# Optimization experiments

Hardware: AMD Instinct MI355X
Metric: run time of the kernel (lower is better)

The kernel has to match this reference:

```python
import jax, jax.numpy as jnp
import numpy as np

V, E, H, L = 10000, 300, 256, 9   # vocab, embed_dim, hidden_dim, num_labels
B, T = 128, 512                   # batch, seq_len


def setup_inputs() -> dict:
    key = jax.random.key(0)
    ks = jax.random.split(key, 14)
    s = 0.05
    emb = jax.random.normal(ks[2], (V, E), jnp.float32) * s
    emb = emb.at[0].set(0.0)  # padding_idx=0
    return {
        "input_ids": jax.random.randint(ks[0], (B, T), 0, V),
        "attention_mask": jnp.ones((B, T), jnp.int32),
        "labels": jax.random.randint(ks[1], (B, T), 0, L),
        "emb": emb,
        "Wih_f": jax.random.normal(ks[3], (4 * H, E), jnp.float32) * s,
        "Whh_f": jax.random.normal(ks[4], (4 * H, H), jnp.float32) * s,
        "b_f": jnp.zeros((4 * H,), jnp.float32),
        "Wih_b": jax.random.normal(ks[5], (4 * H, E), jnp.float32) * s,
        "Whh_b": jax.random.normal(ks[6], (4 * H, H), jnp.float32) * s,
        "b_b": jnp.zeros((4 * H,), jnp.float32),
        "Wc": jax.random.normal(ks[7], (L, 2 * H), jnp.float32) * s,
        "bc": jnp.zeros((L,), jnp.float32),
        "transitions": jax.random.normal(ks[8], (L, L), jnp.float32) * 0.1,
        "start_trans": jax.random.normal(ks[9], (L,), jnp.float32) * 0.1,
        "end_trans": jax.random.normal(ks[10], (L,), jnp.float32) * 0.1,
    }


def _lstm_dir(x, Wih, Whh, b):
    # x: (T, B, E) -> hidden states (T, B, H); PyTorch gate order i,f,g,o
    Bn = x.shape[1]
    h0 = jnp.zeros((Bn, Whh.shape[1]), x.dtype)
    c0 = jnp.zeros((Bn, Whh.shape[1]), x.dtype)
    # precompute input projections once (big GEMM), scan only does small HxH GEMM
    xp = jnp.einsum('tbe,ge->tbg', x, Wih) + b
    def step(carry, xg):
        h, c = carry
        g = xg + h @ Whh.T
        i, f, gg, o = jnp.split(g, 4, axis=-1)
        c = jax.nn.sigmoid(f) * c + jax.nn.sigmoid(i) * jnp.tanh(gg)
        h = jax.nn.sigmoid(o) * jnp.tanh(c)
        return (h, c), h
    _, hs = jax.lax.scan(step, (h0, c0), xp)
    return hs


def reference(input_ids, attention_mask, labels, emb, Wih_f, Whh_f, b_f,
              Wih_b, Whh_b, b_b, Wc, bc, transitions, start_trans, end_trans):
    x = emb[input_ids]                       # (B, T, E)
    xt = jnp.transpose(x, (1, 0, 2))         # (T, B, E)
    hf = _lstm_dir(xt, Wih_f, Whh_f, b_f)
    hb = _lstm_dir(xt[::-1], Wih_b, Whh_b, b_b)[::-1]
    h = jnp.concatenate([hf, hb], axis=-1)   # (T, B, 2H); dropout is identity in eval
    em = h @ Wc.T + bc                       # (T, B, L) emissions

    mask = jnp.transpose(attention_mask, (1, 0)).astype(bool)  # (T, B)
    tags = jnp.transpose(labels, (1, 0))                        # (T, B)
    Bn = em.shape[1]
    bidx = jnp.arange(Bn)

    # --- numerator: score of gold path (torchcrf._compute_score) ---
    score0 = start_trans[tags[0]] + em[0, bidx, tags[0]]
    def num_step(carry, inp):
        score, prev = carry
        e_t, t_t, m_t = inp
        score = score + (transitions[prev, t_t] + e_t[bidx, t_t]) * m_t
        return (score, t_t), None
    (score, _), _ = jax.lax.scan(
        num_step, (score0, tags[0]),
        (em[1:], tags[1:], mask[1:].astype(em.dtype)))
    seq_ends = mask.astype(jnp.int32).sum(0) - 1
    last_tags = tags[seq_ends, bidx]
    score = score + end_trans[last_tags]

    # --- denominator: log partition (torchcrf._compute_normalizer) ---
    alpha0 = start_trans + em[0]             # (B, L)
    def den_step(alpha, inp):
        e_t, m_t = inp
        nxt = jax.nn.logsumexp(alpha[:, :, None] + transitions[None] + e_t[:, None, :], axis=1)
        return jnp.where(m_t[:, None], nxt, alpha), None
    alpha, _ = jax.lax.scan(den_step, alpha0, (em[1:], mask[1:]))
    logZ = jax.nn.logsumexp(alpha + end_trans, axis=-1)

    llh = score - logZ
    return -jnp.mean(llh)  # crf(..., reduction='mean'), negated
```

## Files before the change

kernel.cpp:

```cpp
#include <hip/hip_runtime.h>
#include <hip/hip_bf16.h>
#include <hip/hip_fp16.h>

#define Vn 10000
#define En 300
#define E2n 150
#define Hn 256
#define Gn 1024
#define Ln 9
#define Bn 128
#define Tn 512

#if defined(__has_builtin)
#  if __has_builtin(__builtin_amdgcn_sdot8)
#    define HAS_SDOT8 1
#  endif
#endif
#ifndef HAS_SDOT8
#  define HAS_SDOT8 0
#endif

typedef _Float16 half2_t __attribute__((ext_vector_type(2)));

static __device__ __forceinline__ float bf2f(unsigned short u) {
    return __uint_as_float(((unsigned int)u) << 16);
}
static __device__ __forceinline__ unsigned short f2bf(float f) {
    unsigned int x = __float_as_uint(f);
    return (unsigned short)((x + 0x7FFFu + ((x >> 16) & 1u)) >> 16);
}
static __device__ __forceinline__ float sigm(float x) {
    return 1.f / (1.f + __expf(-x));
}
static __device__ __forceinline__ float tanh_fast(float x) {
    return 2.f / (1.f + __expf(-2.f * x)) - 1.f;
}
static __device__ __forceinline__ int dot8(unsigned int w, int h, int acc) {
#if HAS_SDOT8
    return __builtin_amdgcn_sdot8((int)w, h, acc, false);
#else
    unsigned int wl = ((w & 0x0F0F0F0Fu) ^ 0x08080808u) - 0x08080808u;
    unsigned int wh = (((w >> 4) & 0x0F0F0F0Fu) ^ 0x08080808u) - 0x08080808u;
    unsigned int hl = (((unsigned)h & 0x0F0F0F0Fu) ^ 0x08080808u) - 0x08080808u;
    unsigned int hh = ((((unsigned)h >> 4) & 0x0F0F0F0Fu) ^ 0x08080808u) - 0x08080808u;
    acc = __builtin_amdgcn_sdot4((int)wl, (int)hl, acc, false);
    return __builtin_amdgcn_sdot4((int)wh, (int)hh, acc, false);
#endif
}
static __device__ __forceinline__ unsigned int packf16(float a, float b) {
    half2_t v = {(_Float16)a, (_Float16)b};
    return __builtin_bit_cast(unsigned int, v);
}
static __device__ __forceinline__ half2_t h2(unsigned int u) {
    return __builtin_bit_cast(half2_t, u);
}

#define NPREP_A 5860
#define NPREP_B 1200
#define NPREP_C 512

__global__ __launch_bounds__(256) void k_prep(
    const float* __restrict__ emb, unsigned int* __restrict__ embp,
    const float* __restrict__ Wih_f, const float* __restrict__ Wih_b,
    unsigned int* __restrict__ WT16_f, unsigned int* __restrict__ WT16_b,
    const float* __restrict__ Whh_f, const float* __restrict__ Whh_b,
    unsigned int* __restrict__ qr_f, unsigned int* __restrict__ ql_f,
    unsigned int* __restrict__ qr_b, unsigned int* __restrict__ ql_b,
    float* __restrict__ scl_f, float* __restrict__ scl_b) {
    int bx = blockIdx.x, tid = threadIdx.x;
    if (bx < NPREP_A) {
        int n = bx * 256 + tid;
        if (n < Vn * E2n) {
            int v = n / E2n, e2 = n % E2n;
            embp[n] = packf16(emb[(size_t)v * En + 2 * e2],
                              emb[(size_t)v * En + 2 * e2 + 1]);
        }
        return;
    }
    if (bx < NPREP_A + NPREP_B) {
        int m = (bx - NPREP_A) * 256 + tid;
        int dir = m / 153600;
        int n = m % 153600;
        const float* src = dir ? Wih_b : Wih_f;
        unsigned int* dst = dir ? WT16_b : WT16_f;
        int e2 = n / Gn, j = n % Gn;
        dst[n] = packf16(src[(size_t)j * En + 2 * e2],
                         src[(size_t)j * En + 2 * e2 + 1]);
        return;
    }
    int idx = (bx - NPREP_A - NPREP_B) * 4 + (tid >> 6);
    int dir = idx >> 10;
    int j = idx & 1023;
    int lane = tid & 63;
    const float* W = dir ? Whh_b : Whh_f;
    float w8[8];
    float m = 0.f;
    if (lane < 32) {
        float4 wlo = *(const float4*)&W[(size_t)j * Hn + 8 * lane];
        float4 whi = *(const float4*)&W[(size_t)j * Hn + 8 * lane + 4];
        w8[0] = wlo.x; w8[1] = wlo.y; w8[2] = wlo.z; w8[3] = wlo.w;
        w8[4] = whi.x; w8[5] = whi.y; w8[6] = whi.z; w8[7] = whi.w;
        #pragma unroll
        for (int i = 0; i < 8; ++i) m = fmaxf(m, fabsf(w8[i]));
    }
    #pragma unroll
    for (int sft = 32; sft >= 1; sft >>= 1) m = fmaxf(m, __shfl_xor(m, sft, 64));
    float inv = (m > 0.f) ? (7.f / m) : 0.f;
    if (lane < 32) {
        unsigned int d = 0;
        #pragma unroll
        for (int i = 0; i < 8; ++i) {
            int qi = (int)rintf(w8[i] * inv);
            d |= ((unsigned int)(qi & 0xF)) << (4 * i);
        }
        if (lane < 24)
            (dir ? qr_b : qr_f)[(size_t)((lane >> 2) * 1024 + j) * 4 + (lane & 3)] = d;
        else {
            int e = lane - 24;
            (dir ? ql_b : ql_f)[(size_t)((e >> 2) * 1024 + j) * 4 + (e & 3)] = d;
        }
    }
    if (lane == 0) (dir ? scl_b : scl_f)[j] = m / 49.f;
}

__global__ __launch_bounds__(256) void k_proj(
    const unsigned int* __restrict__ embp,
    const unsigned int* __restrict__ WT16_f, const unsigned int* __restrict__ WT16_b,
    const float* __restrict__ b_f, const float* __restrict__ b_b,
    unsigned short* __restrict__ Pf, unsigned short* __restrict__ Pb) {
    int tid = threadIdx.x;
    int tx = tid & 63, ty = tid >> 6;
    int dir = blockIdx.z;
    const unsigned int* WT = dir ? WT16_b : WT16_f;
    const float* bias = dir ? b_b : b_f;
    unsigned short* P = dir ? Pb : Pf;
    int v0 = blockIdx.x * 32 + ty * 8;
    int j0 = blockIdx.y * 256 + tx * 4;
    int vr[8];
    #pragma unroll
    for (int r = 0; r < 8; ++r) { int v = v0 + r; vr[r] = (v < Vn) ? v : Vn - 1; }
    half2_t ax[8], ay[8], az[8], aw[8];
    #pragma unroll
    for (int r = 0; r < 8; ++r) {
        half2_t z = {(_Float16)0.f, (_Float16)0.f};
        ax[r] = z; ay[r] = z; az[r] = z; aw[r] = z;
    }
    for (int e2 = 0; e2 < E2n; e2 += 2) {
        uint4 w0 = *(const uint4*)&WT[(size_t)(e2 + 0) * Gn + j0];
        uint4 w1 = *(const uint4*)&WT[(size_t)(e2 + 1) * Gn + j0];
        #pragma unroll
        for (int r = 0; r < 8; ++r) {
            uint2 a = *(const uint2*)&embp[(size_t)vr[r] * E2n + e2];
            half2_t a0 = h2(a.x), a1 = h2(a.y);
            ax[r] += a0 * h2(w0.x); ay[r] += a0 * h2(w0.y);
            az[r] += a0 * h2(w0.z); aw[r] += a0 * h2(w0.w);
            ax[r] += a1 * h2(w1.x); ay[r] += a1 * h2(w1.y);
            az[r] += a1 * h2(w1.z); aw[r] += a1 * h2(w1.w);
        }
    }
    float4 bb = *(const float4*)&bias[j0];
    #pragma unroll
    for (int r = 0; r < 8; ++r) {
        if (v0 + r < Vn) {
            ushort4 o;
            o.x = f2bf((float)ax[r].x + (float)ax[r].y + bb.x);
            o.y = f2bf((float)ay[r].x + (float)ay[r].y + bb.y);
            o.z = f2bf((float)az[r].x + (float)az[r].y + bb.z);
            o.w = f2bf((float)aw[r].x + (float)aw[r].y + bb.w);
            *(ushort4*)&P[(size_t)(v0 + r) * Gn + j0] = o;
        }
    }
}

__global__ __launch_bounds__(1024, 4) void k_lstm(
    const int* __restrict__ ids,
    const uint4* __restrict__ qr_f, const uint4* __restrict__ ql_f,
    const uint4* __restrict__ qr_b, const uint4* __restrict__ ql_b,
    const float* __restrict__ scl_f, const float* __restrict__ scl_b,
    const unsigned short* __restrict__ Pf, const unsigned short* __restrict__ Pb,
    unsigned short* __restrict__ hs_f, unsigned short* __restrict__ hs_b) {
    __shared__ uint4 wlds[2 * 1024];
    __shared__ float g_stage[Gn];
    __shared__ uint4 h4v[8];
    __shared__ int ids_lds[Tn];
    int tid = threadIdx.x;
    int dir = blockIdx.x >> 7;
    int batch = blockIdx.x & 127;
    const uint4* qr = dir ? qr_b : qr_f;
    const uint4* ql = dir ? ql_b : ql_f;
    const unsigned short* P = dir ? Pb : Pf;
    unsigned short* hs = dir ? hs_b : hs_f;

    unsigned int wReg[24];
    #pragma unroll
    for (int d4 = 0; d4 < 6; ++d4) {
        uint4 v = qr[(size_t)d4 * 1024 + tid];
        wReg[4*d4+0] = v.x; wReg[4*d4+1] = v.y; wReg[4*d4+2] = v.z; wReg[4*d4+3] = v.w;
    }
    wlds[tid] = ql[tid];
    wlds[1024 + tid] = ql[1024 + tid];
    float sc = (dir ? scl_b : scl_f)[tid];
    if (tid < Tn) ids_lds[tid] = ids[batch * Tn + tid];
    if (tid < 8) { uint4 z = {0u, 0u, 0u, 0u}; h4v[tid] = z; }
    float c = 0.f;
    __syncthreads();

    int t0 = dir ? (Tn - 1) : 0;
    float p = bf2f(P[(size_t)ids_lds[t0] * Gn + tid]);

    for (int s = 0; s < Tn; ++s) {
        asm volatile("" : "+v"(wReg[0]), "+v"(wReg[1]), "+v"(wReg[2]), "+v"(wReg[3]),
                          "+v"(wReg[4]), "+v"(wReg[5]), "+v"(wReg[6]), "+v"(wReg[7]),
                          "+v"(wReg[8]), "+v"(wReg[9]), "+v"(wReg[10]), "+v"(wReg[11]));
        asm volatile("" : "+v"(wReg[12]), "+v"(wReg[13]), "+v"(wReg[14]), "+v"(wReg[15]),
                          "+v"(wReg[16]), "+v"(wReg[17]), "+v"(wReg[18]), "+v"(wReg[19]),
                          "+v"(wReg[20]), "+v"(wReg[21]), "+v"(wReg[22]), "+v"(wReg[23]));

        int t = dir ? (Tn - 1 - s) : s;
        int s2 = (s + 1 < Tn) ? s + 1 : Tn - 1;
        int t2 = dir ? (Tn - 1 - s2) : s2;
        unsigned short nx = P[(size_t)ids_lds[t2] * Gn + tid];

        uint4 hq  = h4v[tid & 7];
        uint4 wv0 = wlds[tid];
        uint4 wv1 = wlds[1024 + tid];

        int a0 = 0, a1 = 0, a2 = 0, a3 = 0;
        #pragma unroll
        for (int g = 0; g < 6; ++g) {
            int h0 = __builtin_amdgcn_readlane((int)hq.x, g);
            int h1 = __builtin_amdgcn_readlane((int)hq.y, g);
            int h2v = __builtin_amdgcn_readlane((int)hq.z, g);
            int h3 = __builtin_amdgcn_readlane((int)hq.w, g);
            a0 = dot8(wReg[4*g+0], h0, a0);
            a1 = dot8(wReg[4*g+1], h1, a1);
            a2 = dot8(wReg[4*g+2], h2v, a2);
            a3 = dot8(wReg[4*g+3], h3, a3);
        }
        {
            int h0 = __builtin_amdgcn_readlane((int)hq.x, 6);
            int h1 = __builtin_amdgcn_readlane((int)hq.y, 6);
            int h2v = __builtin_amdgcn_readlane((int)hq.z, 6);
            int h3 = __builtin_amdgcn_readlane((int)hq.w, 6);
            a0 = dot8(wv0.x, h0, a0);
            a1 = dot8(wv0.y, h1, a1);
            a2 = dot8(wv0.z, h2v, a2);
            a3 = dot8(wv0.w, h3, a3);
            h0 = __builtin_amdgcn_readlane((int)hq.x, 7);
            h1 = __builtin_amdgcn_readlane((int)hq.y, 7);
            h2v = __builtin_amdgcn_readlane((int)hq.z, 7);
            h3 = __builtin_amdgcn_readlane((int)hq.w, 7);
            a0 = dot8(wv1.x, h0, a0);
            a1 = dot8(wv1.y, h1, a1);
            a2 = dot8(wv1.z, h2v, a2);
            a3 = dot8(wv1.w, h3, a3);
        }
        g_stage[tid] = sc * (float)((a0 + a1) + (a2 + a3)) + p;
        __syncthreads();
        if (tid < Hn) {
            float gi = g_stage[tid];
            float gf = g_stage[tid + 256];
            float gg = g_stage[tid + 512];
            float go = g_stage[tid + 768];
            float cn = sigm(gf) * c + sigm(gi) * tanh_fast(gg);
            float hn = sigm(go) * tanh_fast(cn);
            c = cn;
            hs[(size_t)(t * Bn + batch) * Hn + tid] = f2bf(hn);
            int qh = (int)rintf(7.f * hn);
            int qo = __shfl_xor(qh, 1, 64);
            if ((tid & 1) == 0)
                ((char*)h4v)[tid >> 1] = (char)((qh & 0xF) | ((qo & 0xF) << 4));
        }
        __syncthreads();
        p = bf2f(nx);
    }
}

__global__ __launch_bounds__(256) void k_emit(
    const unsigned short* __restrict__ hs_f, const unsigned short* __restrict__ hs_b,
    const float* __restrict__ Wc, const float* __restrict__ bc,
    float* __restrict__ em) {
    __shared__ float wc_s[Ln * 2 * Hn];
    int tid = threadIdx.x;
    for (int i = tid; i < Ln * 2 * Hn; i += 256) wc_s[i] = Wc[i];
    __syncthreads();
    int lane = tid & 63, wid = tid >> 6;
    int tb0 = blockIdx.x * 16 + wid * 4;
    for (int i = 0; i < 4; ++i) {
        int tb = tb0 + i;
        const unsigned short* hf = hs_f + (size_t)tb * Hn;
        const unsigned short* hb = hs_b + (size_t)tb * Hn;
        uint2 uf = *(const uint2*)&hf[lane * 4];
        uint2 ub = *(const uint2*)&hb[lane * 4];
        float f0 = __uint_as_float(uf.x << 16), f1 = __uint_as_float(uf.x & 0xFFFF0000u);
        float f2v = __uint_as_float(uf.y << 16), f3 = __uint_as_float(uf.y & 0xFFFF0000u);
        float b0 = __uint_as_float(ub.x << 16), b1 = __uint_as_float(ub.x & 0xFFFF0000u);
        float b2 = __uint_as_float(ub.y << 16), b3 = __uint_as_float(ub.y & 0xFFFF0000u);
        #pragma unroll
        for (int l = 0; l < Ln; ++l) {
            const float* w = &wc_s[l * 2 * Hn];
            float pe = f0 * w[4 * lane] + f1 * w[4 * lane + 1]
                     + f2v * w[4 * lane + 2] + f3 * w[4 * lane + 3]
                     + b0 * w[Hn + 4 * lane] + b1 * w[Hn + 4 * lane + 1]
                     + b2 * w[Hn + 4 * lane + 2] + b3 * w[Hn + 4 * lane + 3];
            #pragma unroll
            for (int m = 32; m >= 1; m >>= 1) pe += __shfl_xor(pe, m, 64);
            if (lane == 0) em[(size_t)tb * Ln + l] = pe + bc[l];
        }
    }
}

__global__ __launch_bounds__(64) void k_crf(
    const float* __restrict__ em, const int* __restrict__ labels,
    const int* __restrict__ mask, const float* __restrict__ trans,
    const float* __restrict__ start, const float* __restrict__ endt,
    float* __restrict__ score, float* __restrict__ logZ) {
    int lane = threadIdx.x;
    if (blockIdx.x >= 64) {
        int b = blockIdx.x - 64;
        float acc = 0.f; int cnt = 0;
        for (int t = lane; t < Tn; t += 64) {
            int tag = labels[b * Tn + t];
            int mt = mask[b * Tn + t];
            cnt += mt;
            float e = em[(size_t)(t * Bn + b) * Ln + tag];
            if (t == 0) {
                acc += start[tag] + e;
            } else {
                int prev = labels[b * Tn + t - 1];
                if (mt) acc += trans[prev * Ln + tag] + e;
            }
        }
        #pragma unroll
        for (int m = 32; m >= 1; m >>= 1) {
            acc += __shfl_xor(acc, m, 64);
            cnt += __shfl_xor(cnt, m, 64);
        }
        if (lane == 0) {
            int send = cnt - 1;
            int last = labels[b * Tn + send];
            score[b] = acc + endt[last];
        }
        return;
    }
    int grp = lane >> 5;
    int b = blockIdx.x + 64 * grp;
    int lj = lane & 31;
    int jj = (lj < Ln) ? lj : Ln - 1;
    int base = lane & 32;
    float trj[Ln];
    #pragma unroll
    for (int i = 0; i < Ln; ++i) trj[i] = trans[i * Ln + jj];
    float alpha = start[jj] + em[(size_t)b * Ln + jj];
    float e1 = em[(size_t)(1 * Bn + b) * Ln + jj];
    float e2 = em[(size_t)(2 * Bn + b) * Ln + jj];
    int m1 = mask[b * Tn + 1];
    int m2 = mask[b * Tn + 2];
    for (int t = 1; t < Tn; ++t) {
        float s0 = __shfl(alpha, base + 0, 64) + trj[0];
        float s1 = __shfl(alpha, base + 1, 64) + trj[1];
        float s2 = __shfl(alpha, base + 2, 64) + trj[2];
        float s3 = __shfl(alpha, base + 3, 64) + trj[3];
        float s4 = __shfl(alpha, base + 4, 64) + trj[4];
        float s5 = __shfl(alpha, base + 5, 64) + trj[5];
        float s6 = __shfl(alpha, base + 6, 64) + trj[6];
        float s7 = __shfl(alpha, base + 7, 64) + trj[7];
        float s8 = __shfl(alpha, base + 8, 64) + trj[8];
        float mx = fmaxf(fmaxf(fmaxf(s0, s1), fmaxf(s2, s3)),
                         fmaxf(fmaxf(s4, s5), fmaxf(fmaxf(s6, s7), s8)));
        float sum = __expf(s0 - mx) + __expf(s1 - mx) + __expf(s2 - mx)
                  + __expf(s3 - mx) + __expf(s4 - mx) + __expf(s5 - mx)
                  + __expf(s6 - mx) + __expf(s7 - mx) + __expf(s8 - mx);
        float nxt = mx + __logf(sum) + e1;
        if (m1) alpha = nxt;
        e1 = e2; m1 = m2;
        int t2 = (t + 2 < Tn) ? t + 2 : Tn - 1;
        e2 = em[(size_t)(t2 * Bn + b) * Ln + jj];
        m2 = mask[b * Tn + t2];
    }
    float s = (lj < Ln) ? alpha + endt[lj] : -1e30f;
    float mx = s;
    #pragma unroll
    for (int d = 16; d >= 1; d >>= 1) mx = fmaxf(mx, __shfl_xor(mx, d, 64));
    float sm = __expf(s - mx);
    #pragma unroll
    for (int d = 16; d >= 1; d >>= 1) sm += __shfl_xor(sm, d, 64);
    if (lj == 0) logZ[b] = mx + __logf(sm);
}

__global__ __launch_bounds__(128) void k_final(
    const float* __restrict__ score, const float* __restrict__ logZ,
    float* __restrict__ out) {
    __shared__ float s_s[128];
    int tid = threadIdx.x;
    s_s[tid] = score[tid] - logZ[tid];
    #pragma unroll
    for (int m = 64; m >= 1; m >>= 1) {
        __syncthreads();
        if (tid < m) s_s[tid] += s_s[tid + m];
    }
    if (tid == 0) out[0] = -s_s[0] / (float)Bn;
}

extern "C" void kernel_launch(void* const* d_in, const int* in_sizes, int n_in,
                              void* d_out, int out_size, void* d_ws, size_t ws_size,
                              hipStream_t stream) {
    const int* ids = (const int*)d_in[0];
    const int* msk = (const int*)d_in[1];
    const int* lbl = (const int*)d_in[2];
    const float* emb = (const float*)d_in[3];
    const float* Wih_f = (const float*)d_in[4];
    const float* Whh_f = (const float*)d_in[5];
    const float* b_f = (const float*)d_in[6];
    const float* Wih_b = (const float*)d_in[7];
    const float* Whh_b = (const float*)d_in[8];
    const float* b_b = (const float*)d_in[9];
    const float* Wc = (const float*)d_in[10];
    const float* bc = (const float*)d_in[11];
    const float* trans = (const float*)d_in[12];
    const float* st = (const float*)d_in[13];
    const float* en = (const float*)d_in[14];

    char* ws = (char*)d_ws;
    unsigned int* WT16_f = (unsigned int*)ws;   ws += (size_t)E2n * Gn * 4;
    unsigned int* WT16_b = (unsigned int*)ws;   ws += (size_t)E2n * Gn * 4;
    unsigned int* qr_f = (unsigned int*)ws;     ws += 98304;
    unsigned int* ql_f = (unsigned int*)ws;     ws += 32768;
    unsigned int* qr_b = (unsigned int*)ws;     ws += 98304;
    unsigned int* ql_b = (unsigned int*)ws;     ws += 32768;
    float* scl_f = (float*)ws;                  ws += 4096;
    float* scl_b = (float*)ws;                  ws += 4096;
    unsigned short* Pf = (unsigned short*)ws;   ws += (size_t)Vn * Gn * 2;
    unsigned short* Pb = (unsigned short*)ws;   ws += (size_t)Vn * Gn * 2;
    unsigned short* hs_f = (unsigned short*)ws; ws += (size_t)Tn * Bn * Hn * 2;
    unsigned short* hs_b = (unsigned short*)ws; ws += (size_t)Tn * Bn * Hn * 2;
    float* em = (float*)ws;                     ws += (size_t)Tn * Bn * Ln * 4;
    float* score = (float*)ws;                  ws += 512;
    float* logZ = (float*)ws;                   ws += 512;
    unsigned int* embp = (unsigned int*)hs_f;

    k_prep<<<NPREP_A + NPREP_B + NPREP_C, 256, 0, stream>>>(
        emb, embp, Wih_f, Wih_b, WT16_f, WT16_b,
        Whh_f, Whh_b, qr_f, ql_f, qr_b, ql_b, scl_f, scl_b);
    k_proj<<<dim3(313, 4, 2), 256, 0, stream>>>(embp, WT16_f, WT16_b, b_f, b_b, Pf, Pb);
    k_lstm<<<256, 1024, 0, stream>>>(ids,
        (const uint4*)qr_f, (const uint4*)ql_f, (const uint4*)qr_b, (const uint4*)ql_b,
        scl_f, scl_b, Pf, Pb, hs_f, hs_b);
    k_emit<<<4096, 256, 0, stream>>>(hs_f, hs_b, Wc, bc, em);
    k_crf<<<192, 64, 0, stream>>>(em, lbl, msk, trans, st, en, score, logZ);
    k_final<<<1, 128, 0, stream>>>(score, logZ, (float*)d_out);
}
```

Baseline: 909.3 us.

## Fuse embedding fp16 packing into projection GEMM and widen column tile

Drops the prep pass that converted the embedding table to packed fp16. The projection kernel now reads fp32 embedding rows directly and converts them in registers. Each thread also computes 8 output columns instead of 4, which halves the grid's y dimension and doubles reuse of each loaded embedding row. This removes one full read and write of the embedding table, at the cost of more register pressure (64 half2 accumulators) and per-element conversion inside the GEMM loop.

After: 952.1 us. +4.7%, slower.

```diff
diff --git a/kernel.cpp b/kernel.cpp
--- a/kernel.cpp
+++ b/kernel.cpp
@@ -55,12 +55,10 @@
     return __builtin_bit_cast(half2_t, u);
 }
 
-#define NPREP_A 5860
 #define NPREP_B 1200
 #define NPREP_C 512
 
 __global__ __launch_bounds__(256) void k_prep(
-    const float* __restrict__ emb, unsigned int* __restrict__ embp,
     const float* __restrict__ Wih_f, const float* __restrict__ Wih_b,
     unsigned int* __restrict__ WT16_f, unsigned int* __restrict__ WT16_b,
     const float* __restrict__ Whh_f, const float* __restrict__ Whh_b,
@@ -68,17 +66,8 @@
     unsigned int* __restrict__ qr_b, unsigned int* __restrict__ ql_b,
     float* __restrict__ scl_f, float* __restrict__ scl_b) {
     int bx = blockIdx.x, tid = threadIdx.x;
-    if (bx < NPREP_A) {
-        int n = bx * 256 + tid;
-        if (n < Vn * E2n) {
-            int v = n / E2n, e2 = n % E2n;
-            embp[n] = packf16(emb[(size_t)v * En + 2 * e2],
-                              emb[(size_t)v * En + 2 * e2 + 1]);
-        }
-        return;
-    }
-    if (bx < NPREP_A + NPREP_B) {
-        int m = (bx - NPREP_A) * 256 + tid;
+    if (bx < NPREP_B) {
+        int m = bx * 256 + tid;
         int dir = m / 153600;
         int n = m % 153600;
         const float* src = dir ? Wih_b : Wih_f;
@@ -88,7 +77,7 @@
                          src[(size_t)j * En + 2 * e2 + 1]);
         return;
     }
-    int idx = (bx - NPREP_A - NPREP_B) * 4 + (tid >> 6);
+    int idx = (bx - NPREP_B) * 4 + (tid >> 6);
     int dir = idx >> 10;
     int j = idx & 1023;
     int lane = tid & 63;
@@ -124,7 +113,7 @@
 }
 
 __global__ __launch_bounds__(256) void k_proj(
-    const unsigned int* __restrict__ embp,
+    const float* __restrict__ emb,
     const unsigned int* __restrict__ WT16_f, const unsigned int* __restrict__ WT16_b,
     const float* __restrict__ b_f, const float* __restrict__ b_b,
     unsigned short* __restrict__ Pf, unsigned short* __restrict__ Pb) {
@@ -135,39 +124,51 @@
     const float* bias = dir ? b_b : b_f;
     unsigned short* P = dir ? Pb : Pf;
     int v0 = blockIdx.x * 32 + ty * 8;
-    int j0 = blockIdx.y * 256 + tx * 4;
+    int j0 = blockIdx.y * 512 + tx * 8;
     int vr[8];
     #pragma unroll
     for (int r = 0; r < 8; ++r) { int v = v0 + r; vr[r] = (v < Vn) ? v : Vn - 1; }
-    half2_t ax[8], ay[8], az[8], aw[8];
-    #pragma unroll
-    for (int r = 0; r < 8; ++r) {
-        half2_t z = {(_Float16)0.f, (_Float16)0.f};
-        ax[r] = z; ay[r] = z; az[r] = z; aw[r] = z;
-    }
+    half2_t acc[8][8];
+    #pragma unroll
+    for (int r = 0; r < 8; ++r)
+        #pragma unroll
+        for (int j = 0; j < 8; ++j) {
+            half2_t z = {(_Float16)0.f, (_Float16)0.f};
+            acc[r][j] = z;
+        }
     for (int e2 = 0; e2 < E2n; e2 += 2) {
-        uint4 w0 = *(const uint4*)&WT[(size_t)(e2 + 0) * Gn + j0];
-        uint4 w1 = *(const uint4*)&WT[(size_t)(e2 + 1) * Gn + j0];
+        uint4 w0a = *(const uint4*)&WT[(size_t)e2 * Gn + j0];
+        uint4 w0b = *(const uint4*)&WT[(size_t)e2 * Gn + j0 + 4];
+        uint4 w1a = *(const uint4*)&WT[(size_t)(e2 + 1) * Gn + j0];
+        uint4 w1b = *(const uint4*)&WT[(size_t)(e2 + 1) * Gn + j0 + 4];
+        unsigned int w0[8] = {w0a.x, w0a.y, w0a.z, w0a.w, w0b.x, w0b.y, w0b.z, w0b.w};
+        unsigned int w1[8] = {w1a.x, w1a.y, w1a.z, w1a.w, w1b.x, w1b.y, w1b.z, w1b.w};
         #pragma unroll
         for (int r = 0; r < 8; ++r) {
-            uint2 a = *(const uint2*)&embp[(size_t)vr[r] * E2n + e2];
-            half2_t a0 = h2(a.x), a1 = h2(a.y);
-            ax[r] += a0 * h2(w0.x); ay[r] += a0 * h2(w0.y);
-            az[r] += a0 * h2(w0.z); aw[r] += a0 * h2(w0.w);
-            ax[r] += a1 * h2(w1.x); ay[r] += a1 * h2(w1.y);
-            az[r] += a1 * h2(w1.z); aw[r] += a1 * h2(w1.w);
-        }
-    }
-    float4 bb = *(const float4*)&bias[j0];
+            float4 a = *(const float4*)&emb[(size_t)vr[r] * En + 2 * e2];
+            half2_t alo = {(_Float16)a.x, (_Float16)a.y};
+            half2_t ahi = {(_Float16)a.z, (_Float16)a.w};
+            #pragma unroll
+            for (int j = 0; j < 8; ++j) {
+                acc[r][j] += alo * h2(w0[j]);
+                acc[r][j] += ahi * h2(w1[j]);
+            }
+        }
+    }
     #pragma unroll
     for (int r = 0; r < 8; ++r) {
         if (v0 + r < Vn) {
-            ushort4 o;
-            o.x = f2bf((float)ax[r].x + (float)ax[r].y + bb.x);
-            o.y = f2bf((float)ay[r].x + (float)ay[r].y + bb.y);
-            o.z = f2bf((float)az[r].x + (float)az[r].y + bb.z);
-            o.w = f2bf((float)aw[r].x + (float)aw[r].y + bb.w);
-            *(ushort4*)&P[(size_t)(v0 + r) * Gn + j0] = o;
+            ushort4 o0, o1;
+            o0.x = f2bf((float)acc[r][0].x + (float)acc[r][0].y + bias[j0 + 0]);
+            o0.y = f2bf((float)acc[r][1].x + (float)acc[r][1].y + bias[j0 + 1]);
+            o0.z = f2bf((float)acc[r][2].x + (float)acc[r][2].y + bias[j0 + 2]);
+            o0.w = f2bf((float)acc[r][3].x + (float)acc[r][3].y + bias[j0 + 3]);
+            o1.x = f2bf((float)acc[r][4].x + (float)acc[r][4].y + bias[j0 + 4]);
+            o1.y = f2bf((float)acc[r][5].x + (float)acc[r][5].y + bias[j0 + 5]);
+            o1.z = f2bf((float)acc[r][6].x + (float)acc[r][6].y + bias[j0 + 6]);
+            o1.w = f2bf((float)acc[r][7].x + (float)acc[r][7].y + bias[j0 + 7]);
+            *(ushort4*)&P[(size_t)(v0 + r) * Gn + j0] = o0;
+            *(ushort4*)&P[(size_t)(v0 + r) * Gn + j0 + 4] = o1;
         }
     }
 }
@@ -437,12 +438,11 @@
     float* em = (float*)ws;                     ws += (size_t)Tn * Bn * Ln * 4;
     float* score = (float*)ws;                  ws += 512;
     float* logZ = (float*)ws;                   ws += 512;
-    unsigned int* embp = (unsigned int*)hs_f;
-
-    k_prep<<<NPREP_A + NPREP_B + NPREP_C, 256, 0, stream>>>(
-        emb, embp, Wih_f, Wih_b, WT16_f, WT16_b,
+
+    k_prep<<<NPREP_B + NPREP_C, 256, 0, stream>>>(
+        Wih_f, Wih_b, WT16_f, WT16_b,
         Whh_f, Whh_b, qr_f, ql_f, qr_b, ql_b, scl_f, scl_b);
-    k_proj<<<dim3(313, 4, 2), 256, 0, stream>>>(embp, WT16_f, WT16_b, b_f, b_b, Pf, Pb);
+    k_proj<<<dim3(313, 2, 2), 256, 0, stream>>>(emb, WT16_f, WT16_b, b_f, b_b, Pf, Pb);
     k_lstm<<<256, 1024, 0, stream>>>(ids,
         (const uint4*)qr_f, (const uint4*)ql_f, (const uint4*)qr_b, (const uint4*)ql_b,
         scl_f, scl_b, Pf, Pb, hs_f, hs_b);
```
